# Optimization experiments

Hardware: AMD Instinct MI355X
Metric: run time of the kernel (lower is better)

## Reference

```python
import jax, jax.numpy as jnp
import numpy as np

B, S, D = 2, 1024, 1024
E = 8          # routed experts
I = 1024       # per-expert intermediate
IS = 1024      # shared expert intermediate
TOP_K = 2
NUM_SHARED = 1


def setup_inputs() -> dict:
    key = jax.random.key(0)
    ks = jax.random.split(key, 8)
    scale = 0.02
    return {
        "x": jax.random.normal(ks[0], (B, S, D), dtype=jnp.float32),
        "w_gate": jax.random.normal(ks[1], (D, E), dtype=jnp.float32) * scale,
        "wg": jax.random.normal(ks[2], (E, D, I), dtype=jnp.float32) * scale,  # expert gate_proj
        "wu": jax.random.normal(ks[3], (E, D, I), dtype=jnp.float32) * scale,  # expert up_proj
        "wd": jax.random.normal(ks[4], (E, I, D), dtype=jnp.float32) * scale,  # expert down_proj
        "ws_g": jax.random.normal(ks[5], (NUM_SHARED, D, IS), dtype=jnp.float32) * scale,
        "ws_u": jax.random.normal(ks[6], (NUM_SHARED, D, IS), dtype=jnp.float32) * scale,
        "ws_d": jax.random.normal(ks[7], (NUM_SHARED, IS, D), dtype=jnp.float32) * scale,
    }


def _swiglu(t, w_gate_proj, w_up, w_down):
    # t: [N, D]
    g = t @ w_gate_proj            # [N, I]
    u = t @ w_up                   # [N, I]
    return (jax.nn.silu(g) * u) @ w_down  # [N, D]


def reference(x, w_gate, wg, wu, wd, ws_g, ws_u, ws_d):
    Bb, Ss, Dd = x.shape
    x_flat = x.reshape(Bb * Ss, Dd)                  # [N, D]
    N = x_flat.shape[0]

    # --- router ---
    logits = x_flat @ w_gate                          # [N, E]
    topk_logits, topk_idx = jax.lax.top_k(logits, TOP_K)
    topk_w = jax.nn.softmax(topk_logits, axis=-1)     # [N, K]

    # --- aux load-balancing loss ---
    one_hot = jax.nn.one_hot(topk_idx, E, dtype=jnp.float32)  # [N, K, E]
    f = one_hot.sum(axis=1).mean(axis=0)                       # [E]
    P = jax.nn.softmax(logits, axis=-1).mean(axis=0)           # [E]
    aux_loss = E * jnp.sum(f * P)

    # --- combine weights: cw[n, e] = sum_k topk_w[n,k] * 1[topk_idx[n,k]==e] ---
    cw = jnp.einsum("nk,nke->ne", topk_w, one_hot)             # [N, E]

    # --- routed experts: dense compute over all experts, weighted combine ---
    g = jnp.einsum("nd,edi->eni", x_flat, wg)                  # [E, N, I]
    u = jnp.einsum("nd,edi->eni", x_flat, wu)                  # [E, N, I]
    a = jax.nn.silu(g) * u                                     # [E, N, I]
    y = jnp.einsum("eni,eid->end", a, wd)                      # [E, N, D]
    routed = jnp.einsum("ne,end->nd", cw, y)                   # [N, D]

    # --- shared experts ---
    shared = jnp.zeros_like(x_flat)
    for s in range(NUM_SHARED):
        shared = shared + _swiglu(x_flat, ws_g[s], ws_u[s], ws_d[s])

    out = (routed + shared).reshape(Bb, Ss, Dd)
    return out, aux_loss
```

## Files before the change

kernel.cpp:

```cpp
#include <hip/hip_runtime.h>
#include <math.h>

typedef unsigned short u16;
typedef __attribute__((ext_vector_type(8))) short short8;
typedef __attribute__((ext_vector_type(4))) float f32x4;
typedef __attribute__((ext_vector_type(4))) unsigned short u16x4;
typedef __attribute__((ext_vector_type(8))) unsigned short u16x8;

#define N_TOK 2048
#define DIM 1024
#define OUT_ELEMS 2097152

#define GLDS16(gp, lp) __builtin_amdgcn_global_load_lds( \
    (const __attribute__((address_space(1))) unsigned int*)(gp), \
    (__attribute__((address_space(3))) unsigned int*)(lp), 16, 0, 0)

__device__ __forceinline__ u16 f2bf(float f) {
    union { float f; unsigned u; } v; v.f = f;
    unsigned r = (v.u + 0x7FFFu + ((v.u >> 16) & 1u)) >> 16;
    return (u16)r;
}
__device__ __forceinline__ float bf2f(u16 h) {
    union { unsigned u; float f; } v; v.u = ((unsigned)h) << 16;
    return v.f;
}

__global__ void k_init(int* __restrict__ tlist, int* __restrict__ curs,
                       float* __restrict__ Psum, int* __restrict__ cnt8) {
    int i = blockIdx.x * 256 + threadIdx.x;
    tlist[4096 + i] = i;
    if (i < 16) curs[i] = 0;
    if (i < 8) { Psum[i] = 0.f; cnt8[i] = 0; }
}

__global__ void k_cvt_w(const float* __restrict__ wg, const float* __restrict__ wu,
                        const float* __restrict__ wd, const float* __restrict__ wsg,
                        const float* __restrict__ wsu, const float* __restrict__ wsd,
                        u16* __restrict__ wgt, u16* __restrict__ wut,
                        u16* __restrict__ wdt, u16* __restrict__ wsgt,
                        u16* __restrict__ wsut, u16* __restrict__ wsdt) {
    __shared__ u16 tile[128 * 136];
    int bx = blockIdx.x;
    int mat = bx >> 6;
    int tl  = bx & 63;
    int tr = tl >> 3, tc = tl & 7;
    const float* src; u16* dst;
    if      (mat <  8) { src = wg  + (size_t)mat * 1048576;        dst = wgt + (size_t)mat * 1048576; }
    else if (mat < 16) { src = wu  + (size_t)(mat - 8) * 1048576;  dst = wut + (size_t)(mat - 8) * 1048576; }
    else if (mat < 24) { src = wd  + (size_t)(mat - 16) * 1048576; dst = wdt + (size_t)(mat - 16) * 1048576; }
    else if (mat == 24){ src = wsg; dst = wsgt; }
    else if (mat == 25){ src = wsu; dst = wsut; }
    else               { src = wsd; dst = wsdt; }
    int t = threadIdx.x;
    int col = (t & 31) * 4;
    int rb  = t >> 5;
    const float* sp = src + (size_t)(tr * 128) * 1024 + tc * 128 + col;

    f32x4 v[16];
#pragma unroll
    for (int j = 0; j < 16; j++)
        v[j] = *(const f32x4*)(sp + (size_t)(j * 8 + rb) * 1024);
#pragma unroll
    for (int j = 0; j < 16; j++) {
        int row = j * 8 + rb;
        u16x4 o;
        o.x = f2bf(v[j].x); o.y = f2bf(v[j].y); o.z = f2bf(v[j].z); o.w = f2bf(v[j].w);
        *(u16x4*)(tile + row * 136 + col) = o;
    }
    __syncthreads();
    int n  = t & 127;
    int kb = (t >> 7) * 64;
    u16* drow = dst + (size_t)(tc * 128 + n) * 1024 + tr * 128;
#pragma unroll
    for (int j = 0; j < 8; j++) {
        int kc = kb + j * 8;
        u16x8 o;
#pragma unroll
        for (int i = 0; i < 8; i++) o[i] = tile[(kc + i) * 136 + n];
        *(u16x8*)(drow + kc) = o;
    }
}

__global__ void k_router(const float* __restrict__ x, const float* __restrict__ wgate,
                         u16* __restrict__ xb, int* __restrict__ tidx,
                         float* __restrict__ tw, float* __restrict__ Psum,
                         int* __restrict__ cnt8) {
    __shared__ float sP[8];
    __shared__ int   sC[8];
    int t = threadIdx.x;
    if (t < 8) { sP[t] = 0.f; sC[t] = 0; }
    __syncthreads();
    int wave = t >> 6;
    int lane = t & 63;
    int n = blockIdx.x * 4 + wave;
    const float* xr = x + (size_t)n * DIM;
    u16* xbr = xb + (size_t)n * DIM;
    float acc[8] = {0.f,0.f,0.f,0.f,0.f,0.f,0.f,0.f};
#pragma unroll
    for (int i = 0; i < 16; i++) {
        int d = lane + i * 64;
        float xv = xr[d];
        xbr[d] = f2bf(xv);
        const float* wr = wgate + d * 8;
#pragma unroll
        for (int e = 0; e < 8; e++) acc[e] += xv * wr[e];
    }
#pragma unroll
    for (int off = 32; off; off >>= 1) {
#pragma unroll
        for (int e = 0; e < 8; e++) acc[e] += __shfl_xor(acc[e], off);
    }
    if (lane == 0) {
        float mx = acc[0];
#pragma unroll
        for (int e = 1; e < 8; e++) mx = fmaxf(mx, acc[e]);
        float p[8], s = 0.f;
#pragma unroll
        for (int e = 0; e < 8; e++) { p[e] = expf(acc[e] - mx); s += p[e]; }
        float inv = 1.f / s;
#pragma unroll
        for (int e = 0; e < 8; e++) atomicAdd(&sP[e], p[e] * inv);
        int i0 = 0; float b0 = acc[0];
#pragma unroll
        for (int e = 1; e < 8; e++) if (acc[e] > b0) { b0 = acc[e]; i0 = e; }
        int i1 = -1; float b1 = -3.4e38f;
#pragma unroll
        for (int e = 0; e < 8; e++) if (e != i0 && acc[e] > b1) { b1 = acc[e]; i1 = e; }
        float w0 = 1.f / (1.f + expf(b1 - b0));
        tidx[n * 2] = i0; tidx[n * 2 + 1] = i1;
        tw[n * 2] = w0;   tw[n * 2 + 1] = 1.f - w0;
        atomicAdd(&sC[i0], 1);
        atomicAdd(&sC[i1], 1);
    }
    __syncthreads();
    if (t < 8) {
        atomicAdd(&Psum[t], sP[t]);
        atomicAdd(&cnt8[t], sC[t]);
    }
}

__global__ void k_scatter(const int* __restrict__ tidx, const float* __restrict__ Psum,
                          const int* __restrict__ cnt8, int* __restrict__ curs,
                          int* __restrict__ tlist, int* __restrict__ slots,
                          float* __restrict__ out, int* __restrict__ counts,
                          int* __restrict__ offs) {
    __shared__ int s_off[8];
    int t = threadIdx.x;
    if (t == 0) {
        int o = 0;
        for (int e = 0; e < 8; e++) { s_off[e] = o; o += cnt8[e]; }
    }
    __syncthreads();
    if (blockIdx.x == 0 && t == 0) {
        float aux = 0.f;
        for (int e = 0; e < 8; e++) {
            int c = cnt8[e];
            aux += (float)c * Psum[e];
            offs[e] = s_off[e]; counts[e] = c;
        }
        out[OUT_ELEMS] = 8.f * aux / ((float)N_TOK * (float)N_TOK);
        offs[8] = 4096; counts[8] = 2048;
    }
    int n = blockIdx.x * 256 + t;
    if (n < N_TOK) {
#pragma unroll
        for (int k = 0; k < 2; k++) {
            int e = tidx[n * 2 + k];
            int p = atomicAdd(&curs[e], 1);
            int sl = s_off[e] + p;
            tlist[sl] = n;
            slots[n * 2 + k] = sl;
        }
    }
}

__global__ __launch_bounds__(256, 2)
void k_gemm1(const u16* __restrict__ xb, const u16* __restrict__ wgt,
             const u16* __restrict__ wut, const u16* __restrict__ wsgt,
             const u16* __restrict__ wsut, const int* __restrict__ tlist,
             const int* __restrict__ counts, const int* __restrict__ offs,
             u16* __restrict__ H) {
    int bx = blockIdx.x;
    int job = bx >> 7;
    int mt = (bx >> 3) & 15;
    int nt = bx & 7;
    int jcnt = counts[job];
    int m0 = mt << 7;
    if (m0 >= jcnt) return;
    int joff = offs[job];
    int n0 = nt << 7;
    const u16* Bg = (job < 8) ? (wgt + (size_t)job * 1048576) : wsgt;
    const u16* Bu = (job < 8) ? (wut + (size_t)job * 1048576) : wsut;

    __shared__ __attribute__((aligned(128))) u16 As[4096];
    __shared__ __attribute__((aligned(128))) u16 Bgs[4096];
    __shared__ __attribute__((aligned(128))) u16 Bus[4096];

    int t = threadIdx.x;
    int wave = t >> 6, lane = t & 63;
    int ch = (lane & 3) * 8;
    int r0 = (wave * 2 + 0) * 16 + (lane >> 2);
    int r1 = (wave * 2 + 1) * 16 + (lane >> 2);
    int tok0 = tlist[joff + m0 + r0];
    int tok1 = tlist[joff + m0 + r1];
    const u16* a0 = xb + (size_t)tok0 * 1024 + ch;
    const u16* a1 = xb + (size_t)tok1 * 1024 + ch;
    const u16* g0 = Bg + (size_t)(n0 + r0) * 1024 + ch;
    const u16* g1 = Bg + (size_t)(n0 + r1) * 1024 + ch;
    const u16* u0 = Bu + (size_t)(n0 + r0) * 1024 + ch;
    const u16* u1 = Bu + (size_t)(n0 + r1) * 1024 + ch;
    u16* lA0 = As  + (wave * 2 + 0) * 512;  u16* lA1 = As  + (wave * 2 + 1) * 512;
    u16* lG0 = Bgs + (wave * 2 + 0) * 512;  u16* lG1 = Bgs + (wave * 2 + 1) * 512;
    u16* lU0 = Bus + (wave * 2 + 0) * 512;  u16* lU1 = Bus + (wave * 2 + 1) * 512;

    int wm = (wave >> 1) << 6, wn = (wave & 1) << 6;
    int quad = lane >> 4, lr = lane & 15;

    f32x4 accg[4][4], accu[4][4];
    f32x4 zz = {0.f, 0.f, 0.f, 0.f};
#pragma unroll
    for (int i = 0; i < 4; i++)
#pragma unroll
        for (int j = 0; j < 4; j++) { accg[i][j] = zz; accu[i][j] = zz; }

    for (int k0 = 0; k0 < 1024; k0 += 32) {
        GLDS16(a0 + k0, lA0);  GLDS16(a1 + k0, lA1);
        GLDS16(g0 + k0, lG0);  GLDS16(g1 + k0, lG1);
        GLDS16(u0 + k0, lU0);  GLDS16(u1 + k0, lU1);
        __syncthreads();
        short8 af[4], bgf[4], buf[4];
#pragma unroll
        for (int i = 0; i < 4; i++) {
            af[i]  = *(const short8*)(As  + (wm + i * 16 + lr) * 32 + quad * 8);
            bgf[i] = *(const short8*)(Bgs + (wn + i * 16 + lr) * 32 + quad * 8);
            buf[i] = *(const short8*)(Bus + (wn + i * 16 + lr) * 32 + quad * 8);
        }
#pragma unroll
        for (int mi = 0; mi < 4; mi++)
#pragma unroll
            for (int ni = 0; ni < 4; ni++) {
                accg[mi][ni] = __builtin_amdgcn_mfma_f32_16x16x32_bf16(af[mi], bgf[ni], accg[mi][ni], 0, 0, 0);
                accu[mi][ni] = __builtin_amdgcn_mfma_f32_16x16x32_bf16(af[mi], buf[ni], accu[mi][ni], 0, 0, 0);
            }
        __syncthreads();
    }
#pragma unroll
    for (int mi = 0; mi < 4; mi++) {
        int rowb = m0 + wm + mi * 16 + quad * 4;
#pragma unroll
        for (int rr = 0; rr < 4; rr++) {
            int row = rowb + rr;
            if (row < jcnt) {
                size_t base = (size_t)(joff + row) * 1024 + n0 + wn;
#pragma unroll
                for (int ni = 0; ni < 4; ni++) {
                    float g = accg[mi][ni][rr];
                    float u = accu[mi][ni][rr];
                    float h = (g / (1.f + expf(-g))) * u;
                    H[base + ni * 16 + lr] = f2bf(h);
                }
            }
        }
    }
}

__global__ __launch_bounds__(256, 2)
void k_gemm2(const u16* __restrict__ H, const u16* __restrict__ wdt,
             const u16* __restrict__ wsdt, const int* __restrict__ counts,
             const int* __restrict__ offs, u16* __restrict__ Y) {
    int bx = blockIdx.x;
    int job = bx >> 7;
    int mt = (bx >> 3) & 15;
    int nt = bx & 7;
    int jcnt = counts[job];
    int m0 = mt << 7;
    if (m0 >= jcnt) return;
    int joff = offs[job];
    int n0 = nt << 7;
    const u16* Bt = (job < 8) ? (wdt + (size_t)job * 1048576) : wsdt;

    __shared__ __attribute__((aligned(128))) u16 As[4096];
    __shared__ __attribute__((aligned(128))) u16 Bs[4096];

    int t = threadIdx.x;
    int wave = t >> 6, lane = t & 63;
    int ch = (lane & 3) * 8;
    int r0 = (wave * 2 + 0) * 16 + (lane >> 2);
    int r1 = (wave * 2 + 1) * 16 + (lane >> 2);
    const u16* a0 = H + (size_t)(joff + m0 + r0) * 1024 + ch;
    const u16* a1 = H + (size_t)(joff + m0 + r1) * 1024 + ch;
    const u16* b0 = Bt + (size_t)(n0 + r0) * 1024 + ch;
    const u16* b1 = Bt + (size_t)(n0 + r1) * 1024 + ch;
    u16* lA0 = As + (wave * 2 + 0) * 512;  u16* lA1 = As + (wave * 2 + 1) * 512;
    u16* lB0 = Bs + (wave * 2 + 0) * 512;  u16* lB1 = Bs + (wave * 2 + 1) * 512;

    int wm = (wave >> 1) << 6, wn = (wave & 1) << 6;
    int quad = lane >> 4, lr = lane & 15;

    f32x4 acc[4][4];
    f32x4 zz = {0.f, 0.f, 0.f, 0.f};
#pragma unroll
    for (int i = 0; i < 4; i++)
#pragma unroll
        for (int j = 0; j < 4; j++) acc[i][j] = zz;

    for (int k0 = 0; k0 < 1024; k0 += 32) {
        GLDS16(a0 + k0, lA0);  GLDS16(a1 + k0, lA1);
        GLDS16(b0 + k0, lB0);  GLDS16(b1 + k0, lB1);
        __syncthreads();
        short8 af[4], bf[4];
#pragma unroll
        for (int i = 0; i < 4; i++) {
            af[i] = *(const short8*)(As + (wm + i * 16 + lr) * 32 + quad * 8);
            bf[i] = *(const short8*)(Bs + (wn + i * 16 + lr) * 32 + quad * 8);
        }
#pragma unroll
        for (int mi = 0; mi < 4; mi++)
#pragma unroll
            for (int ni = 0; ni < 4; ni++)
                acc[mi][ni] = __builtin_amdgcn_mfma_f32_16x16x32_bf16(af[mi], bf[ni], acc[mi][ni], 0, 0, 0);
        __syncthreads();
    }
#pragma unroll
    for (int mi = 0; mi < 4; mi++) {
        int rowb = m0 + wm + mi * 16 + quad * 4;
#pragma unroll
        for (int rr = 0; rr < 4; rr++) {
            int row = rowb + rr;
            if (row < jcnt) {
                u16* yrow = Y + (size_t)(joff + row) * 1024 + n0 + wn;
#pragma unroll
                for (int ni = 0; ni < 4; ni++)
                    yrow[ni * 16 + lr] = f2bf(acc[mi][ni][rr]);
            }
        }
    }
}

__global__ void k_combine(const u16* __restrict__ Y, const int* __restrict__ slots,
                          const float* __restrict__ tw, float* __restrict__ out) {
    int n = blockIdx.x;
    int d = threadIdx.x;
    int s0 = slots[n * 2], s1 = slots[n * 2 + 1];
    float w0 = tw[n * 2], w1 = tw[n * 2 + 1];
    u16x4 y0 = ((const u16x4*)(Y + (size_t)s0 * 1024))[d];
    u16x4 y1 = ((const u16x4*)(Y + (size_t)s1 * 1024))[d];
    u16x4 ys = ((const u16x4*)(Y + (size_t)(4096 + n) * 1024))[d];
    f32x4 r;
    r.x = w0 * bf2f(y0.x) + w1 * bf2f(y1.x) + bf2f(ys.x);
    r.y = w0 * bf2f(y0.y) + w1 * bf2f(y1.y) + bf2f(ys.y);
    r.z = w0 * bf2f(y0.z) + w1 * bf2f(y1.z) + bf2f(ys.z);
    r.w = w0 * bf2f(y0.w) + w1 * bf2f(y1.w) + bf2f(ys.w);
    ((f32x4*)(out + (size_t)n * 1024))[d] = r;
}

extern "C" void kernel_launch(void* const* d_in, const int* in_sizes, int n_in,
                              void* d_out, int out_size, void* d_ws, size_t ws_size,
                              hipStream_t stream) {
    const float* x     = (const float*)d_in[0];
    const float* wgate = (const float*)d_in[1];
    const float* wg    = (const float*)d_in[2];
    const float* wu    = (const float*)d_in[3];
    const float* wd    = (const float*)d_in[4];
    const float* wsg   = (const float*)d_in[5];
    const float* wsu   = (const float*)d_in[6];
    const float* wsd   = (const float*)d_in[7];
    float* out = (float*)d_out;

    char* ws = (char*)d_ws;
    u16*   xb    = (u16*)(ws + 0);
    u16*   wgt   = (u16*)(ws + 4194304);
    u16*   wut   = (u16*)(ws + 20971520);
    u16*   wdt   = (u16*)(ws + 37748736);
    u16*   wsgt  = (u16*)(ws + 54525952);
    u16*   wsut  = (u16*)(ws + 56623104);
    u16*   wsdt  = (u16*)(ws + 58720256);
    u16*   H     = (u16*)(ws + 60817408);
    u16*   Y     = (u16*)(ws + 4194304);
    int*   tidx  = (int*)(ws + 73400320);
    float* tw    = (float*)(ws + 73416704);
    int*   tlist = (int*)(ws + 73433088);
    int*   slots = (int*)(ws + 73457664);
    int*   counts= (int*)(ws + 73474048);
    int*   offs  = (int*)(ws + 73474112);
    int*   curs  = (int*)(ws + 73474176);
    float* Psum  = (float*)(ws + 73474240);
    int*   cnt8  = (int*)(ws + 73474304);

    k_init<<<8, 256, 0, stream>>>(tlist, curs, Psum, cnt8);
    k_router<<<512, 256, 0, stream>>>(x, wgate, xb, tidx, tw, Psum, cnt8);
    k_scatter<<<8, 256, 0, stream>>>(tidx, Psum, cnt8, curs, tlist, slots,
                                     out, counts, offs);
    k_cvt_w<<<1728, 256, 0, stream>>>(wg, wu, wd, wsg, wsu, wsd,
                                      wgt, wut, wdt, wsgt, wsut, wsdt);
    k_gemm1<<<1152, 256, 0, stream>>>(xb, wgt, wut, wsgt, wsut, tlist, counts, offs, H);
    k_gemm2<<<1152, 256, 0, stream>>>(H, wdt, wsdt, counts, offs, Y);
    k_combine<<<2048, 256, 0, stream>>>(Y, slots, tw, out);
}
```

Before: 279.6 us.

## Store converted bf16 weights in k-blocked layout for contiguous B-tile loads

The weight conversion kernel now writes weights as 8-element K-groups laid out consecutively along N, not as a full transpose. The GEMM kernels then load B tiles as contiguous 1KB runs per wave and read LDS fragments with the matching quad-major indexing. This replaces the tiled transpose in the converter, which had strided LDS reads, with a simpler chunked reorder and makes the global loads for B more contiguous. The LDS fragment read pattern changes, which may introduce bank conflicts.

```diff
diff --git a/kernel.cpp b/kernel.cpp
--- a/kernel.cpp
+++ b/kernel.cpp
@@ -39,11 +39,10 @@
                         u16* __restrict__ wgt, u16* __restrict__ wut,
                         u16* __restrict__ wdt, u16* __restrict__ wsgt,
                         u16* __restrict__ wsut, u16* __restrict__ wsdt) {
-    __shared__ u16 tile[128 * 136];
+    __shared__ u16 tile[8 * 1024];
     int bx = blockIdx.x;
-    int mat = bx >> 6;
-    int tl  = bx & 63;
-    int tr = tl >> 3, tc = tl & 7;
+    int mat = bx >> 7;
+    int chunk = bx & 127;
     const float* src; u16* dst;
     if      (mat <  8) { src = wg  + (size_t)mat * 1048576;        dst = wgt + (size_t)mat * 1048576; }
     else if (mat < 16) { src = wu  + (size_t)(mat - 8) * 1048576;  dst = wut + (size_t)(mat - 8) * 1048576; }
@@ -51,33 +50,29 @@
     else if (mat == 24){ src = wsg; dst = wsgt; }
     else if (mat == 25){ src = wsu; dst = wsut; }
     else               { src = wsd; dst = wsdt; }
-    int t = threadIdx.x;
-    int col = (t & 31) * 4;
-    int rb  = t >> 5;
-    const float* sp = src + (size_t)(tr * 128) * 1024 + tc * 128 + col;
-
-    f32x4 v[16];
-#pragma unroll
-    for (int j = 0; j < 16; j++)
-        v[j] = *(const f32x4*)(sp + (size_t)(j * 8 + rb) * 1024);
-#pragma unroll
-    for (int j = 0; j < 16; j++) {
-        int row = j * 8 + rb;
+    const float* srow = src + (size_t)chunk * 8192;
+    u16* dchunk = dst + (size_t)chunk * 8192;
+    int t = threadIdx.x;
+    int r  = t >> 5;
+    int c0 = (t & 31) * 4;
+    f32x4 v[8];
+#pragma unroll
+    for (int j = 0; j < 8; j++)
+        v[j] = *(const f32x4*)(srow + r * 1024 + c0 + j * 128);
+#pragma unroll
+    for (int j = 0; j < 8; j++) {
         u16x4 o;
         o.x = f2bf(v[j].x); o.y = f2bf(v[j].y); o.z = f2bf(v[j].z); o.w = f2bf(v[j].w);
-        *(u16x4*)(tile + row * 136 + col) = o;
+        *(u16x4*)(tile + r * 1024 + c0 + j * 128) = o;
     }
     __syncthreads();
-    int n  = t & 127;
-    int kb = (t >> 7) * 64;
-    u16* drow = dst + (size_t)(tc * 128 + n) * 1024 + tr * 128;
-#pragma unroll
-    for (int j = 0; j < 8; j++) {
-        int kc = kb + j * 8;
+#pragma unroll
+    for (int j = 0; j < 4; j++) {
+        int n = t + j * 256;
         u16x8 o;
 #pragma unroll
-        for (int i = 0; i < 8; i++) o[i] = tile[(kc + i) * 136 + n];
-        *(u16x8*)(drow + kc) = o;
+        for (int k = 0; k < 8; k++) o[k] = tile[k * 1024 + n];
+        *(u16x8*)(dchunk + n * 8) = o;
     }
 }
 
@@ -205,13 +200,11 @@
     int tok1 = tlist[joff + m0 + r1];
     const u16* a0 = xb + (size_t)tok0 * 1024 + ch;
     const u16* a1 = xb + (size_t)tok1 * 1024 + ch;
-    const u16* g0 = Bg + (size_t)(n0 + r0) * 1024 + ch;
-    const u16* g1 = Bg + (size_t)(n0 + r1) * 1024 + ch;
-    const u16* u0 = Bu + (size_t)(n0 + r0) * 1024 + ch;
-    const u16* u1 = Bu + (size_t)(n0 + r1) * 1024 + ch;
+    const u16* gB = Bg + (size_t)wave * 8192 + (size_t)(n0 + lane) * 8;
+    const u16* uB = Bu + (size_t)wave * 8192 + (size_t)(n0 + lane) * 8;
     u16* lA0 = As  + (wave * 2 + 0) * 512;  u16* lA1 = As  + (wave * 2 + 1) * 512;
-    u16* lG0 = Bgs + (wave * 2 + 0) * 512;  u16* lG1 = Bgs + (wave * 2 + 1) * 512;
-    u16* lU0 = Bus + (wave * 2 + 0) * 512;  u16* lU1 = Bus + (wave * 2 + 1) * 512;
+    u16* lGa = Bgs + wave * 1024;           u16* lGb = Bgs + wave * 1024 + 512;
+    u16* lUa = Bus + wave * 1024;           u16* lUb = Bus + wave * 1024 + 512;
 
     int wm = (wave >> 1) << 6, wn = (wave & 1) << 6;
     int quad = lane >> 4, lr = lane & 15;
@@ -224,16 +217,18 @@
         for (int j = 0; j < 4; j++) { accg[i][j] = zz; accu[i][j] = zz; }
 
     for (int k0 = 0; k0 < 1024; k0 += 32) {
-        GLDS16(a0 + k0, lA0);  GLDS16(a1 + k0, lA1);
-        GLDS16(g0 + k0, lG0);  GLDS16(g1 + k0, lG1);
-        GLDS16(u0 + k0, lU0);  GLDS16(u1 + k0, lU1);
+        size_t koff = (size_t)k0 * 1024;
+        GLDS16(a0 + k0, lA0);        GLDS16(a1 + k0, lA1);
+        GLDS16(gB + koff, lGa);      GLDS16(gB + koff + 512, lGb);
+        GLDS16(uB + koff, lUa);      GLDS16(uB + koff + 512, lUb);
         __syncthreads();
         short8 af[4], bgf[4], buf[4];
 #pragma unroll
         for (int i = 0; i < 4; i++) {
+            int nrow = wn + i * 16 + lr;
             af[i]  = *(const short8*)(As  + (wm + i * 16 + lr) * 32 + quad * 8);
-            bgf[i] = *(const short8*)(Bgs + (wn + i * 16 + lr) * 32 + quad * 8);
-            buf[i] = *(const short8*)(Bus + (wn + i * 16 + lr) * 32 + quad * 8);
+            bgf[i] = *(const short8*)(Bgs + quad * 1024 + nrow * 8);
+            buf[i] = *(const short8*)(Bus + quad * 1024 + nrow * 8);
         }
 #pragma unroll
         for (int mi = 0; mi < 4; mi++)
@@ -289,10 +284,9 @@
     int r1 = (wave * 2 + 1) * 16 + (lane >> 2);
     const u16* a0 = H + (size_t)(joff + m0 + r0) * 1024 + ch;
     const u16* a1 = H + (size_t)(joff + m0 + r1) * 1024 + ch;
-    const u16* b0 = Bt + (size_t)(n0 + r0) * 1024 + ch;
-    const u16* b1 = Bt + (size_t)(n0 + r1) * 1024 + ch;
+    const u16* bB = Bt + (size_t)wave * 8192 + (size_t)(n0 + lane) * 8;
     u16* lA0 = As + (wave * 2 + 0) * 512;  u16* lA1 = As + (wave * 2 + 1) * 512;
-    u16* lB0 = Bs + (wave * 2 + 0) * 512;  u16* lB1 = Bs + (wave * 2 + 1) * 512;
+    u16* lBa = Bs + wave * 1024;           u16* lBb = Bs + wave * 1024 + 512;
 
     int wm = (wave >> 1) << 6, wn = (wave & 1) << 6;
     int quad = lane >> 4, lr = lane & 15;
@@ -305,14 +299,15 @@
         for (int j = 0; j < 4; j++) acc[i][j] = zz;
 
     for (int k0 = 0; k0 < 1024; k0 += 32) {
-        GLDS16(a0 + k0, lA0);  GLDS16(a1 + k0, lA1);
-        GLDS16(b0 + k0, lB0);  GLDS16(b1 + k0, lB1);
+        size_t koff = (size_t)k0 * 1024;
+        GLDS16(a0 + k0, lA0);    GLDS16(a1 + k0, lA1);
+        GLDS16(bB + koff, lBa);  GLDS16(bB + koff + 512, lBb);
         __syncthreads();
         short8 af[4], bf[4];
 #pragma unroll
         for (int i = 0; i < 4; i++) {
             af[i] = *(const short8*)(As + (wm + i * 16 + lr) * 32 + quad * 8);
-            bf[i] = *(const short8*)(Bs + (wn + i * 16 + lr) * 32 + quad * 8);
+            bf[i] = *(const short8*)(Bs + quad * 1024 + (wn + i * 16 + lr) * 8);
         }
 #pragma unroll
         for (int mi = 0; mi < 4; mi++)
@@ -391,7 +386,7 @@
     k_router<<<512, 256, 0, stream>>>(x, wgate, xb, tidx, tw, Psum, cnt8);
     k_scatter<<<8, 256, 0, stream>>>(tidx, Psum, cnt8, curs, tlist, slots,
                                      out, counts, offs);
-    k_cvt_w<<<1728, 256, 0, stream>>>(wg, wu, wd, wsg, wsu, wsd,
+    k_cvt_w<<<3456, 256, 0, stream>>>(wg, wu, wd, wsg, wsu, wsd,
                                       wgt, wut, wdt, wsgt, wsut, wsdt);
     k_gemm1<<<1152, 256, 0, stream>>>(xb, wgt, wut, wsgt, wsut, tlist, counts, offs, H);
     k_gemm2<<<1152, 256, 0, stream>>>(H, wdt, wsdt, counts, offs, Y);
```

New measurement: 271.3 us. -3.0%, faster.
